# Performance work log

Measured on AMD Instinct MI355X. Metric: run time of the kernel, lower is better.

The kernel has to match this reference:

```python
import jax, jax.numpy as jnp
import numpy as np
import math

B, M, C, H = 4, 2048, 512, 8
DQK = C // 4 // H  # 16 per-head query/key dim


def setup_inputs() -> dict:
    key = jax.random.key(0)
    ks = jax.random.split(key, 8)
    s = 0.02
    return {
        "x": jax.random.normal(ks[0], (B, M, C), dtype=jnp.float32),
        "mask": jax.random.randint(ks[1], (B, M), 0, 2, dtype=jnp.int32),
        "Wq": jax.random.normal(ks[2], (C, C // 4), dtype=jnp.float32) * s,
        "bq": jnp.zeros((C // 4,), dtype=jnp.float32),
        "Wk": jax.random.normal(ks[3], (C, C // 4), dtype=jnp.float32) * s,
        "bk": jnp.zeros((C // 4,), dtype=jnp.float32),
        "Wv": jax.random.normal(ks[4], (C, C), dtype=jnp.float32) * s,
        "bv": jnp.zeros((C,), dtype=jnp.float32),
        "gamma": jnp.ones((1,), dtype=jnp.float32),
    }


def reference(x, mask, Wq, bq, Wk, bk, Wv, bv, gamma):
    b, m, c = x.shape
    # projections, split heads: q/k -> (B, H, M, DQK), v -> (B, H, M, C//H)
    q = (x @ Wq + bq).reshape(b, m, H, -1).transpose(0, 2, 1, 3)
    k = (x @ Wk + bk).reshape(b, m, H, -1).transpose(0, 2, 1, 3)
    v = (x @ Wv + bv).reshape(b, m, H, -1).transpose(0, 2, 1, 3)
    scale = 1.0 / math.sqrt(q.shape[-1])
    scores = jnp.einsum('bhmd,bhnd->bhmn', q, k) * scale
    beta = jax.nn.softmax(jax.nn.relu(scores), axis=-1)  # act='relu' pre-softmax
    # att_drop = 0.0 -> identity
    mf = mask.astype(x.dtype)[:, None, None, :]  # (B,1,1,M)
    beta = beta * mf
    beta = beta / (beta.sum(-1, keepdims=True) + 1e-12)
    o = gamma * jnp.einsum('bhmn,bhnd->bhmd', beta, v)  # (B,H,M,C//H)
    return o.transpose(0, 2, 1, 3).reshape(b, m, c)
```

## Files before the change

kernel.cpp:

```cpp
#include <hip/hip_runtime.h>
#include <hip/hip_bf16.h>

#define MSEQ 2048

typedef __attribute__((ext_vector_type(8))) short short8;
typedef __attribute__((ext_vector_type(4))) short short4v;
typedef __attribute__((ext_vector_type(4))) float f32x4;

static __device__ __forceinline__ short bf16b(float f) {
    __hip_bfloat16 h = __float2bfloat16(f);
    return *reinterpret_cast<short*>(&h);
}

static __device__ __forceinline__ float fast_exp2(float x) {
    float r;
    asm("v_exp_f32 %0, %1" : "=v"(r) : "v"(x));
    return r;
}

static __device__ __forceinline__ f32x4 mfma16(short4v a, short4v b, f32x4 c) {
    return __builtin_amdgcn_mfma_f32_16x16x16bf16_1k(a, b, c, 0, 0, 0);
}

static __device__ __forceinline__ void gl_lds16(const void* g, void* l) {
    __builtin_amdgcn_global_load_lds(
        (const __attribute__((address_space(1))) unsigned int*)g,
        (__attribute__((address_space(3))) unsigned int*)l, 16, 0, 0);
}

__global__ __launch_bounds__(256) void prep_kernel(
    const float* __restrict__ x, unsigned short* __restrict__ xb,
    const float* __restrict__ Wq, const float* __restrict__ Wk,
    const float* __restrict__ Wv, unsigned short* __restrict__ WT,
    const int* __restrict__ mask, unsigned short* __restrict__ maskbf)
{
    __shared__ unsigned short Ts[64*72];
    const int bid = blockIdx.x;
    const int t = threadIdx.x;

    if (bid < 2048) {
        const size_t i = ((size_t)bid * 256 + t) * 8;
        const float4 a = *(const float4*)(x + i);
        const float4 b = *(const float4*)(x + i + 4);
        short8 o;
        o[0]=bf16b(a.x); o[1]=bf16b(a.y); o[2]=bf16b(a.z); o[3]=bf16b(a.w);
        o[4]=bf16b(b.x); o[5]=bf16b(b.y); o[6]=bf16b(b.z); o[7]=bf16b(b.w);
        *(short8*)(xb + i) = o;
        return;
    }
    if (bid == 2144) {
        #pragma unroll
        for (int j = 0; j < 8; ++j) {
            const int4 m4 = *(const int4*)(mask + (t*8 + j)*4);
            short4v o;
            o[0]=bf16b((float)m4.x); o[1]=bf16b((float)m4.y);
            o[2]=bf16b((float)m4.z); o[3]=bf16b((float)m4.w);
            *(short4v*)(maskbf + (t*8 + j)*4) = o;
        }
        return;
    }
    const int idx = bid - 2048;
    const int nt = idx >> 3;
    const int kt = idx & 7;
    const int k0 = kt*64;

    const float* W; int ld, n0;
    if (nt < 2)      { W = Wq; ld = 128; n0 = nt*64; }
    else if (nt < 4) { W = Wk; ld = 128; n0 = (nt-2)*64; }
    else             { W = Wv; ld = 512; n0 = (nt-4)*64; }

    #pragma unroll
    for (int s = 0; s < 4; ++s) {
        const int lin = s*256 + t;
        const int krow = lin >> 4, ng = lin & 15;
        const float4 v = *(const float4*)(W + (size_t)(k0+krow)*ld + n0 + ng*4);
        Ts[(ng*4+0)*72 + krow] = (unsigned short)bf16b(v.x);
        Ts[(ng*4+1)*72 + krow] = (unsigned short)bf16b(v.y);
        Ts[(ng*4+2)*72 + krow] = (unsigned short)bf16b(v.z);
        Ts[(ng*4+3)*72 + krow] = (unsigned short)bf16b(v.w);
    }
    __syncthreads();
    #pragma unroll
    for (int s = 0; s < 2; ++s) {
        const int lin = s*256 + t;
        const int nrow = lin >> 3, kg = lin & 7;
        *(short8*)(WT + (size_t)(nt*64 + nrow)*512 + k0 + kg*8) = *(const short8*)&Ts[nrow*72 + kg*8];
    }
}

__global__ __launch_bounds__(256, 3) void proj_mfma(
    const unsigned short* __restrict__ xb, const unsigned short* __restrict__ WT,
    const float* __restrict__ bq, const float* __restrict__ bk, const float* __restrict__ bv,
    const int* __restrict__ mask,
    unsigned short* __restrict__ Qb, unsigned short* __restrict__ Kb, unsigned short* __restrict__ Vt)
{
    const int g0 = blockIdx.y * 6 + blockIdx.x;
    const int xcd = g0 & 7, idx = g0 >> 3;
    const int nt = idx / 16;
    const int r0 = (xcd * 16 + (idx & 15)) * 64;
    const int n0 = nt * 128;
    const int t = threadIdx.x, w = t >> 6, lane = t & 63, l15 = lane & 15, quad = lane >> 4;
    const int qh = w >> 1, chh = w & 1;

    __shared__ short smem[12288];
    short* As = smem;
    short* Bs = smem + 4096;

    f32x4 acc[2][4];
    #pragma unroll
    for (int i = 0; i < 2; ++i)
        #pragma unroll
        for (int j = 0; j < 4; ++j) acc[i][j] = {0.f,0.f,0.f,0.f};

    const int arow = lane >> 2, akg = lane & 3;

#define PROJ_STAGE(BUFI, KK) {                                                          \
    gl_lds16(xb + (size_t)(r0 + w*16 + arow)*512 + (KK) + akg*8,                        \
             (char*)As + (BUFI)*4096 + w*1024);                                         \
    gl_lds16(WT + (size_t)(n0 + w*16 + arow)*512 + (KK) + akg*8,                        \
             (char*)Bs + (BUFI)*8192 + w*1024);                                         \
    gl_lds16(WT + (size_t)(n0 + 64 + w*16 + arow)*512 + (KK) + akg*8,                   \
             (char*)Bs + (BUFI)*8192 + 4096 + w*1024);                                  \
}

    PROJ_STAGE(0, 0)
    __syncthreads();

    #pragma unroll 2
    for (int kp = 0; kp < 16; ++kp) {
        const int cur = kp & 1;
        if (kp < 15) PROJ_STAGE(cur ^ 1, (kp+1)*32)
        short8 Af[2], Bf[4];
        #pragma unroll
        for (int i = 0; i < 2; ++i)
            Af[i] = *(const short8*)&As[cur*2048 + (qh*32 + i*16 + l15)*32 + quad*8];
        #pragma unroll
        for (int j = 0; j < 4; ++j)
            Bf[j] = *(const short8*)&Bs[cur*4096 + (chh*64 + j*16 + l15)*32 + quad*8];
        #pragma unroll
        for (int i = 0; i < 2; ++i)
            #pragma unroll
            for (int j = 0; j < 4; ++j)
                acc[i][j] = __builtin_amdgcn_mfma_f32_16x16x32_bf16(Af[i], Bf[j], acc[i][j], 0, 0, 0);
        __syncthreads();
    }

    const float* bias = (nt == 0) ? bq : (nt == 1) ? bk : (bv + (nt-2)*128);
    const float kscale = (nt == 1) ? 0.36067376022224085f : 1.0f;
    float bj[4];
    #pragma unroll
    for (int j = 0; j < 4; ++j) bj[j] = bias[chh*64 + j*16 + l15];

    const int bb = r0 >> 11, key0 = r0 & 2047;
    short* Ts = smem;
    if (nt < 2) {
        #pragma unroll
        for (int i = 0; i < 2; ++i)
            #pragma unroll
            for (int j = 0; j < 4; ++j)
                #pragma unroll
                for (int r = 0; r < 4; ++r)
                    Ts[(qh*32 + i*16 + quad*4 + r)*136 + chh*64 + j*16 + l15] =
                        bf16b((acc[i][j][r] + bj[j]) * kscale);
    } else {
        float mv[2][4];
        #pragma unroll
        for (int i = 0; i < 2; ++i)
            #pragma unroll
            for (int r = 0; r < 4; ++r)
                mv[i][r] = (float)mask[bb*MSEQ + key0 + qh*32 + i*16 + quad*4 + r];
        #pragma unroll
        for (int i = 0; i < 2; ++i)
            #pragma unroll
            for (int j = 0; j < 4; ++j)
                #pragma unroll
                for (int r = 0; r < 4; ++r)
                    Ts[(chh*64 + j*16 + l15)*72 + qh*32 + i*16 + quad*4 + r] =
                        bf16b((acc[i][j][r] + bj[j]) * mv[i][r]);
    }
    __syncthreads();

    if (nt < 2) {
        unsigned short* Out = (nt == 0) ? Qb : Kb;
        #pragma unroll
        for (int s = 0; s < 4; ++s) {
            const int lin = s*256 + t, row = lin >> 4, seg = lin & 15;
            *(short8*)(Out + (size_t)(r0+row)*128 + seg*8) = *(const short8*)&Ts[row*136 + seg*8];
        }
    } else {
        const int chBase = (nt-2)*128;
        #pragma unroll
        for (int s = 0; s < 4; ++s) {
            const int lin = s*256 + t, row = lin >> 3, seg = lin & 7;
            *(short8*)(Vt + ((size_t)(bb*512 + chBase + row))*MSEQ + key0 + seg*8) =
                *(const short8*)&Ts[row*72 + seg*8];
        }
    }
#undef PROJ_STAGE
}

__global__ __launch_bounds__(512, 4) void attn_mfma(
    const unsigned short* __restrict__ Qb, const unsigned short* __restrict__ Kb,
    const unsigned short* __restrict__ Vt, const unsigned short* __restrict__ maskbf,
    const float* __restrict__ gamma, float* __restrict__ out)
{
    const int bid = blockIdx.y * 16 + blockIdx.x;
    const int lin = (bid & 7) * 64 + (bid >> 3);
    const int mt = lin & 15, bh = lin >> 4;
    const int b  = bh >> 3, h = bh & 7;
    const int m0 = mt * 128;
    const int t  = threadIdx.x;
    const int w = t >> 6, lane = t & 63, l15 = lane & 15, quad = lane >> 4;
    const int mq = m0 + w*16;

    __shared__ __align__(16) short Ks[2][64*16];
    __shared__ __align__(16) short Vs[2][64*64];
    __shared__ __align__(16) short Msb[2][64];

    const short4v qf = *(const short4v*)(Qb + (size_t)(b*MSEQ + mq + l15)*128 + h*16 + quad*4);

    const unsigned short* Kg = Kb + (size_t)(b*MSEQ + (lane>>1))*128 + h*16
                              + (((lane&1) ^ ((lane>>3)&1))*8);
    const unsigned short* Vg = Vt + (size_t)(b*512 + h*64 + w*8 + (lane>>3))*MSEQ
                              + (((lane&7) ^ ((lane>>3)&7)) * 8);
    const unsigned short* Mgb = maskbf + b*MSEQ + lane*8;

#define ATT_STAGE(BUFI, KN) {                                                        \
    gl_lds16(Vg + (KN), &Vs[BUFI][w*512]);                                           \
    if (w < 2)                   gl_lds16(Kg + (size_t)((KN) + w*32)*128, &Ks[BUFI][w*32*16]); \
    else if (w == 2 && lane < 8) gl_lds16(Mgb + (KN), &Msb[BUFI][0]);                \
}

    const char* KsB = (const char*)&Ks[0][0];
    const char* VsB = (const char*)&Vs[0][0];
    const char* MsB = (const char*)&Msb[0][0];
    const int kofs = l15*32 + (((quad>>1) ^ ((l15>>2)&1))*16) + (quad&1)*8;
    const int mofs = quad*8;
    int vb[4];
    #pragma unroll
    for (int v = 0; v < 4; ++v) {
        const int ch = v*16 + l15;
        vb[v] = ch*128 + (((quad>>1) ^ (ch&7))*16) + (quad&1)*8;
    }

    f32x4 O[4];
    #pragma unroll
    for (int v = 0; v < 4; ++v) O[v] = {0.f,0.f,0.f,0.f};
    f32x4 WS = {0.f,0.f,0.f,0.f};

    ATT_STAGE(0, 0)
    __syncthreads();

    #pragma unroll 2
    for (int kt = 0; kt < 32; ++kt) {
        const int cur = kt & 1;
        if (kt < 31) ATT_STAGE(cur ^ 1, (kt+1)*64)

        const char* Kc = KsB + cur*2048;
        const char* Vc = VsB + cur*8192;
        const char* Mc = MsB + cur*128;

        __builtin_amdgcn_s_setprio(1);
        short4v kfs[4], mkfs[4];
        #pragma unroll
        for (int s = 0; s < 4; ++s) {
            kfs[s]  = *(const short4v*)(Kc + kofs + s*512);
            mkfs[s] = *(const short4v*)(Mc + mofs + s*32);
        }

        #pragma unroll
        for (int s = 0; s < 4; ++s) {
            f32x4 sc = {0.f,0.f,0.f,0.f};
            sc = mfma16(kfs[s], qf, sc);
            const float w0 = fast_exp2(fmaxf(sc[0], 0.f));
            const float w1 = fast_exp2(fmaxf(sc[1], 0.f));
            const float w2 = fast_exp2(fmaxf(sc[2], 0.f));
            const float w3 = fast_exp2(fmaxf(sc[3], 0.f));
            const __hip_bfloat162 p01 = __float22bfloat162_rn(make_float2(w0, w1));
            const __hip_bfloat162 p23 = __float22bfloat162_rn(make_float2(w2, w3));
            unsigned u01, u23;
            __builtin_memcpy(&u01, &p01, 4);
            __builtin_memcpy(&u23, &p23, 4);
            uint2 pku; pku.x = u01; pku.y = u23;
            short4v pf;
            __builtin_memcpy(&pf, &pku, 8);
            WS = mfma16(pf, mkfs[s], WS);
            #pragma unroll
            for (int v = 0; v < 4; ++v) {
                const short4v vf = *(const short4v*)(Vc + (vb[v] ^ (s*32)));
                O[v] = mfma16(pf, vf, O[v]);
            }
        }
        __builtin_amdgcn_s_setprio(0);
        __syncthreads();
    }

    const float g = gamma[0];
    float inv[4];
    #pragma unroll
    for (int r = 0; r < 4; ++r) inv[r] = g / fmaxf(WS[r], 1e-20f);

    float* op = out + (size_t)(b*MSEQ + mq + quad*4)*512 + h*64 + l15;
    #pragma unroll
    for (int r = 0; r < 4; ++r) {
        op[(size_t)r*512 +  0] = O[0][r] * inv[r];
        op[(size_t)r*512 + 16] = O[1][r] * inv[r];
        op[(size_t)r*512 + 32] = O[2][r] * inv[r];
        op[(size_t)r*512 + 48] = O[3][r] * inv[r];
    }
#undef ATT_STAGE
}

extern "C" void kernel_launch(void* const* d_in, const int* in_sizes, int n_in,
                              void* d_out, int out_size, void* d_ws, size_t ws_size,
                              hipStream_t stream) {
    const float* x     = (const float*)d_in[0];
    const int*   mask  = (const int*)  d_in[1];
    const float* Wq    = (const float*)d_in[2];
    const float* bq    = (const float*)d_in[3];
    const float* Wk    = (const float*)d_in[4];
    const float* bk    = (const float*)d_in[5];
    const float* Wv    = (const float*)d_in[6];
    const float* bv    = (const float*)d_in[7];
    const float* gamma = (const float*)d_in[8];
    float* outp = (float*)d_out;

    unsigned short* xb = (unsigned short*)d_ws;
    unsigned short* WT = xb + (size_t)8192*512;
    unsigned short* Qb = WT + (size_t)768*512;
    unsigned short* Kb = Qb + (size_t)8192*128;
    unsigned short* Vt = Kb + (size_t)8192*128;
    unsigned short* maskbf = Vt + (size_t)2048*MSEQ;

    prep_kernel<<<2145, 256, 0, stream>>>(x, xb, Wq, Wk, Wv, WT, mask, maskbf);
    proj_mfma<<<dim3(6, 128), 256, 0, stream>>>(xb, WT, bq, bk, bv, mask, Qb, Kb, Vt);
    attn_mfma<<<dim3(16, 32), 512, 0, stream>>>(Qb, Kb, Vt, maskbf, gamma, outp);
}
```

Before: 148.2 us.

## Process two query row-groups per wave to reuse K/V LDS fragments

Each wave now handles 32 query rows, two 16-row groups, instead of 16, so each attention block covers 256 rows and the grid halves to 256 blocks. V fragments read from LDS are loaded once per step and shared by both groups, and each K/V tile staged into LDS serves twice as many queries. This cuts LDS reads and global K/V traffic per query. The cost is more accumulator registers, a lower occupancy hint (2 blocks per CU instead of 4), and fewer blocks to spread across the GPU's compute units.

```diff
diff --git a/kernel.cpp b/kernel.cpp
--- a/kernel.cpp
+++ b/kernel.cpp
@@ -199,25 +199,28 @@
 #undef PROJ_STAGE
 }
 
-__global__ __launch_bounds__(512, 4) void attn_mfma(
+__global__ __launch_bounds__(512, 2) void attn_mfma(
     const unsigned short* __restrict__ Qb, const unsigned short* __restrict__ Kb,
     const unsigned short* __restrict__ Vt, const unsigned short* __restrict__ maskbf,
     const float* __restrict__ gamma, float* __restrict__ out)
 {
-    const int bid = blockIdx.y * 16 + blockIdx.x;
-    const int lin = (bid & 7) * 64 + (bid >> 3);
-    const int mt = lin & 15, bh = lin >> 4;
+    const int bid = blockIdx.y * 8 + blockIdx.x;
+    const int lin = (bid & 7) * 32 + (bid >> 3);
+    const int mt = lin & 7, bh = lin >> 3;
     const int b  = bh >> 3, h = bh & 7;
-    const int m0 = mt * 128;
+    const int m0 = mt * 256;
     const int t  = threadIdx.x;
     const int w = t >> 6, lane = t & 63, l15 = lane & 15, quad = lane >> 4;
-    const int mq = m0 + w*16;
+    const int mq = m0 + w*32;
 
     __shared__ __align__(16) short Ks[2][64*16];
     __shared__ __align__(16) short Vs[2][64*64];
     __shared__ __align__(16) short Msb[2][64];
 
-    const short4v qf = *(const short4v*)(Qb + (size_t)(b*MSEQ + mq + l15)*128 + h*16 + quad*4);
+    short4v qf[2];
+    #pragma unroll
+    for (int g = 0; g < 2; ++g)
+        qf[g] = *(const short4v*)(Qb + (size_t)(b*MSEQ + mq + g*16 + l15)*128 + h*16 + quad*4);
 
     const unsigned short* Kg = Kb + (size_t)(b*MSEQ + (lane>>1))*128 + h*16
                               + (((lane&1) ^ ((lane>>3)&1))*8);
@@ -243,10 +246,12 @@
         vb[v] = ch*128 + (((quad>>1) ^ (ch&7))*16) + (quad&1)*8;
     }
 
-    f32x4 O[4];
-    #pragma unroll
-    for (int v = 0; v < 4; ++v) O[v] = {0.f,0.f,0.f,0.f};
-    f32x4 WS = {0.f,0.f,0.f,0.f};
+    f32x4 O[2][4];
+    #pragma unroll
+    for (int g = 0; g < 2; ++g)
+        #pragma unroll
+        for (int v = 0; v < 4; ++v) O[g][v] = {0.f,0.f,0.f,0.f};
+    f32x4 WS[2] = {{0.f,0.f,0.f,0.f},{0.f,0.f,0.f,0.f}};
 
     ATT_STAGE(0, 0)
     __syncthreads();
@@ -270,43 +275,50 @@
 
         #pragma unroll
         for (int s = 0; s < 4; ++s) {
-            f32x4 sc = {0.f,0.f,0.f,0.f};
-            sc = mfma16(kfs[s], qf, sc);
-            const float w0 = fast_exp2(fmaxf(sc[0], 0.f));
-            const float w1 = fast_exp2(fmaxf(sc[1], 0.f));
-            const float w2 = fast_exp2(fmaxf(sc[2], 0.f));
-            const float w3 = fast_exp2(fmaxf(sc[3], 0.f));
-            const __hip_bfloat162 p01 = __float22bfloat162_rn(make_float2(w0, w1));
-            const __hip_bfloat162 p23 = __float22bfloat162_rn(make_float2(w2, w3));
-            unsigned u01, u23;
-            __builtin_memcpy(&u01, &p01, 4);
-            __builtin_memcpy(&u23, &p23, 4);
-            uint2 pku; pku.x = u01; pku.y = u23;
-            short4v pf;
-            __builtin_memcpy(&pf, &pku, 8);
-            WS = mfma16(pf, mkfs[s], WS);
-            #pragma unroll
-            for (int v = 0; v < 4; ++v) {
-                const short4v vf = *(const short4v*)(Vc + (vb[v] ^ (s*32)));
-                O[v] = mfma16(pf, vf, O[v]);
+            short4v vfs[4];
+            #pragma unroll
+            for (int v = 0; v < 4; ++v)
+                vfs[v] = *(const short4v*)(Vc + (vb[v] ^ (s*32)));
+            #pragma unroll
+            for (int g = 0; g < 2; ++g) {
+                f32x4 sc = {0.f,0.f,0.f,0.f};
+                sc = mfma16(kfs[s], qf[g], sc);
+                const float w0 = fast_exp2(fmaxf(sc[0], 0.f));
+                const float w1 = fast_exp2(fmaxf(sc[1], 0.f));
+                const float w2 = fast_exp2(fmaxf(sc[2], 0.f));
+                const float w3 = fast_exp2(fmaxf(sc[3], 0.f));
+                const __hip_bfloat162 p01 = __float22bfloat162_rn(make_float2(w0, w1));
+                const __hip_bfloat162 p23 = __float22bfloat162_rn(make_float2(w2, w3));
+                unsigned u01, u23;
+                __builtin_memcpy(&u01, &p01, 4);
+                __builtin_memcpy(&u23, &p23, 4);
+                uint2 pku; pku.x = u01; pku.y = u23;
+                short4v pf;
+                __builtin_memcpy(&pf, &pku, 8);
+                WS[g] = mfma16(pf, mkfs[s], WS[g]);
+                #pragma unroll
+                for (int v = 0; v < 4; ++v)
+                    O[g][v] = mfma16(pf, vfs[v], O[g][v]);
             }
         }
         __builtin_amdgcn_s_setprio(0);
         __syncthreads();
     }
 
-    const float g = gamma[0];
-    float inv[4];
-    #pragma unroll
-    for (int r = 0; r < 4; ++r) inv[r] = g / fmaxf(WS[r], 1e-20f);
-
-    float* op = out + (size_t)(b*MSEQ + mq + quad*4)*512 + h*64 + l15;
-    #pragma unroll
-    for (int r = 0; r < 4; ++r) {
-        op[(size_t)r*512 +  0] = O[0][r] * inv[r];
-        op[(size_t)r*512 + 16] = O[1][r] * inv[r];
-        op[(size_t)r*512 + 32] = O[2][r] * inv[r];
-        op[(size_t)r*512 + 48] = O[3][r] * inv[r];
+    const float gm = gamma[0];
+    #pragma unroll
+    for (int g = 0; g < 2; ++g) {
+        float inv[4];
+        #pragma unroll
+        for (int r = 0; r < 4; ++r) inv[r] = gm / fmaxf(WS[g][r], 1e-20f);
+        float* op = out + (size_t)(b*MSEQ + mq + g*16 + quad*4)*512 + h*64 + l15;
+        #pragma unroll
+        for (int r = 0; r < 4; ++r) {
+            op[(size_t)r*512 +  0] = O[g][0][r] * inv[r];
+            op[(size_t)r*512 + 16] = O[g][1][r] * inv[r];
+            op[(size_t)r*512 + 32] = O[g][2][r] * inv[r];
+            op[(size_t)r*512 + 48] = O[g][3][r] * inv[r];
+        }
     }
 #undef ATT_STAGE
 }
@@ -334,5 +346,5 @@
 
     prep_kernel<<<2145, 256, 0, stream>>>(x, xb, Wq, Wk, Wv, WT, mask, maskbf);
     proj_mfma<<<dim3(6, 128), 256, 0, stream>>>(xb, WT, bq, bk, bv, mask, Qb, Kb, Vt);
-    attn_mfma<<<dim3(16, 32), 512, 0, stream>>>(Qb, Kb, Vt, maskbf, gamma, outp);
-}
+    attn_mfma<<<dim3(8, 32), 512, 0, stream>>>(Qb, Kb, Vt, maskbf, gamma, outp);
+}
```

Measured after the change: 155.2 us. 4.7% more time.
